# Kernel optimization log

Measured on AMD Instinct MI355X. Metric: run time of the kernel, lower is better.

Reference implementation:

```python
import jax, jax.numpy as jnp
import numpy as np

B = 16
N = [4096, 1024, 256, 64, 16]
NF = [1, 16, 32, 64, 128, 256]
DEG = 6
KS = 5
LAT = 32


def spline_conv(x, edge_index, pseudo, W, root, bias):
    """SplineConv: open B-spline, degree 1, dim 3, kernel_size 5, sum aggregation (norm=False).
    x: [Nn, Cin], edge_index: [2, E] (src, dst), pseudo: [E, 3] in [0,1], W: [125, Cin, Cout]."""
    src, dst = edge_index[0], edge_index[1]
    v = pseudo * (KS - 1)                       # degree-1 open spline interval
    lo = jnp.clip(jnp.floor(v), 0.0, KS - 2)
    frac = v - lo                               # [E, 3]
    lo = lo.astype(jnp.int32)
    xs = x[src]                                 # [E, Cin] gather
    strides = jnp.array([1, KS, KS * KS], dtype=jnp.int32)
    msg = jnp.zeros((src.shape[0], W.shape[2]), dtype=x.dtype)
    for s in range(8):                          # (degree+1)^dim = 8 basis products
        bits = np.array([(s >> d) & 1 for d in range(3)], dtype=np.int32)
        basis = jnp.prod(jnp.where(bits[None, :] == 1, frac, 1.0 - frac), axis=1)  # [E]
        kidx = jnp.sum((lo + bits[None, :]) * strides[None, :], axis=1)            # [E]
        Wg = W[kidx]                                                               # [E, Cin, Cout]
        msg = msg + basis[:, None] * jnp.einsum('ei,eio->eo', xs, Wg)
    agg = jax.ops.segment_sum(msg, dst, num_segments=x.shape[0])
    return agg + x @ root + bias


def _fwd(fl, ei):
    (x, ea0, ea1, ea2, ea3, ea4, P01, P12, P23, P34, Pn1, P1n, P43, P32, P21, P10,
     W_c1, r_c1, b_c1, W_c2, r_c2, b_c2, W_c3, r_c3, b_c3, W_c4, r_c4, b_c4, W_c5, r_c5, b_c5,
     W_d5, r_d5, b_d5, W_d4, r_d4, b_d4, W_d3, r_d3, b_d3, W_d2, r_d2, b_d2, W_d1, r_d1, b_d1,
     fce1_w, fce1_b, fce21_w, fce21_b, fce22_w, fce22_b, fcd3_w, fcd3_b, fcd4_w, fcd4_b, eps) = fl
    ei0, ei1, ei2, ei3, ei4 = ei
    elu = jax.nn.elu
    # ---- encoder ----
    h = elu(spline_conv(x, ei0, ea0, W_c1, r_c1, b_c1))
    h = P01 @ h.reshape(B, N[0], NF[1])
    h = elu(spline_conv(h.reshape(-1, NF[1]), ei1, ea1, W_c2, r_c2, b_c2))
    h = P12 @ h.reshape(B, N[1], NF[2])
    h = elu(spline_conv(h.reshape(-1, NF[2]), ei2, ea2, W_c3, r_c3, b_c3))
    h = P23 @ h.reshape(B, N[2], NF[3])
    h = elu(spline_conv(h.reshape(-1, NF[3]), ei3, ea3, W_c4, r_c4, b_c4))
    h = P34 @ h.reshape(B, N[3], NF[4])
    h = elu(spline_conv(h.reshape(-1, NF[4]), ei4, ea4, W_c5, r_c5, b_c5))
    h = (Pn1 @ h.reshape(B, N[4], NF[5])).reshape(B, NF[5])
    # 1x1 convs over [B, C, 1, 1] == dense layers
    h = elu(h @ fce1_w + fce1_b)
    mu = h @ fce21_w + fce21_b
    logvar = h @ fce22_w + fce22_b
    # ---- reparameterize ----
    z = eps * jnp.exp(0.5 * logvar) + mu
    # ---- decoder ----
    h = elu(z @ fcd3_w + fcd3_b)
    h = elu(h @ fcd4_w + fcd4_b)
    h = P1n @ h.reshape(B, 1, NF[5])            # [B, N4, nf5]
    h = elu(spline_conv(h.reshape(-1, NF[5]), ei4, ea4, W_d5, r_d5, b_d5))
    h = P43 @ h.reshape(B, N[4], NF[4])
    h = elu(spline_conv(h.reshape(-1, NF[4]), ei3, ea3, W_d4, r_d4, b_d4))
    h = P32 @ h.reshape(B, N[3], NF[3])
    h = elu(spline_conv(h.reshape(-1, NF[3]), ei2, ea2, W_d3, r_d3, b_d3))
    h = P21 @ h.reshape(B, N[2], NF[2])
    h = elu(spline_conv(h.reshape(-1, NF[2]), ei1, ea1, W_d2, r_d2, b_d2))
    h = P10 @ h.reshape(B, N[1], NF[1])
    h = elu(spline_conv(h.reshape(-1, NF[1]), ei0, ea0, W_d1, r_d1, b_d1))
    recon = h.reshape(B, -1)                    # [B, N0] (nf0 == 1)
    return recon, mu, logvar


def setup_inputs() -> dict:
    key = jax.random.key(0)
    ks = iter(jax.random.split(key, 128))
    def nrm(shape, scale=1.0):
        return jax.random.normal(next(ks), shape, dtype=jnp.float32) * scale
    def edges(n):
        # per-sample random mesh-like connectivity, offset per graph copy
        e = jax.random.randint(next(ks), (2, B, n * DEG), 0, n)
        off = (jnp.arange(B) * n)[None, :, None]
        return (e + off).reshape(2, -1).astype(jnp.int32)
    inp = {}
    inp['x'] = nrm((B * N[0], NF[0]))
    for i in range(5):
        inp[f'ea{i}'] = jax.random.uniform(next(ks), (B * N[i] * DEG, 3), dtype=jnp.float32)
    pools = {'P01': (N[1], N[0]), 'P12': (N[2], N[1]), 'P23': (N[3], N[2]), 'P34': (N[4], N[3]),
             'Pn1': (1, N[4]), 'P1n': (N[4], 1), 'P43': (N[3], N[4]), 'P32': (N[2], N[3]),
             'P21': (N[1], N[2]), 'P10': (N[0], N[1])}
    for k2, (a, b) in pools.items():
        inp[k2] = nrm((a, b), 1.0 / np.sqrt(b))
    def spl(name, ci, co):
        inp[f'W_{name}'] = nrm((KS ** 3, ci, co), 0.1 / np.sqrt(ci))
        inp[f'r_{name}'] = nrm((ci, co), 1.0 / np.sqrt(ci))
        inp[f'b_{name}'] = nrm((co,), 0.01)
    spl('c1', NF[0], NF[1]); spl('c2', NF[1], NF[2]); spl('c3', NF[2], NF[3]); spl('c4', NF[3], NF[4]); spl('c5', NF[4], NF[5])
    spl('d5', NF[5], NF[4]); spl('d4', NF[4], NF[3]); spl('d3', NF[3], NF[2]); spl('d2', NF[2], NF[1]); spl('d1', NF[1], NF[0])
    def lin(name, ci, co):
        inp[f'{name}_w'] = nrm((ci, co), 1.0 / np.sqrt(ci))
        inp[f'{name}_b'] = nrm((co,), 0.01)
    lin('fce1', NF[5], NF[5]); lin('fce21', NF[5], LAT); lin('fce22', NF[5], LAT)
    lin('fcd3', LAT, NF[5]); lin('fcd4', NF[5], NF[5])
    inp['eps'] = nrm((B, LAT))
    for i in range(5):
        inp[f'ei{i}'] = edges(N[i])
    return inp


def reference(x, ea0, ea1, ea2, ea3, ea4, P01, P12, P23, P34, Pn1, P1n, P43, P32, P21, P10,
              W_c1, r_c1, b_c1, W_c2, r_c2, b_c2, W_c3, r_c3, b_c3, W_c4, r_c4, b_c4, W_c5, r_c5, b_c5,
              W_d5, r_d5, b_d5, W_d4, r_d4, b_d4, W_d3, r_d3, b_d3, W_d2, r_d2, b_d2, W_d1, r_d1, b_d1,
              fce1_w, fce1_b, fce21_w, fce21_b, fce22_w, fce22_b, fcd3_w, fcd3_b, fcd4_w, fcd4_b, eps,
              ei0, ei1, ei2, ei3, ei4):
    fl = (x, ea0, ea1, ea2, ea3, ea4, P01, P12, P23, P34, Pn1, P1n, P43, P32, P21, P10,
          W_c1, r_c1, b_c1, W_c2, r_c2, b_c2, W_c3, r_c3, b_c3, W_c4, r_c4, b_c4, W_c5, r_c5, b_c5,
          W_d5, r_d5, b_d5, W_d4, r_d4, b_d4, W_d3, r_d3, b_d3, W_d2, r_d2, b_d2, W_d1, r_d1, b_d1,
          fce1_w, fce1_b, fce21_w, fce21_b, fce22_w, fce22_b, fcd3_w, fcd3_b, fcd4_w, fcd4_b, eps)
    return _fwd(fl, (ei0, ei1, ei2, ei3, ei4))
```

## Files before the change

kernel.cpp:

```cpp
#include <hip/hip_runtime.h>
#include <hip/hip_bf16.h>

#define TPB 256
#define CDIV(a,b) (((a)+(b)-1)/(b))

__device__ __forceinline__ float elu_f(float v) {
    return v > 0.f ? v : expm1f(v);
}

__device__ __forceinline__ int ld_idx(const void* __restrict__ ei, int pos, int is64) {
    if (is64) return (int)((const long long*)ei)[pos];
    return ((const int*)ei)[pos];
}

__device__ __forceinline__ void spline_basis(const float* __restrict__ pseudo, int e,
                                             float bas[8], int kidx[8]) {
    float f[3]; int lo[3];
#pragma unroll
    for (int d = 0; d < 3; ++d) {
        float v = pseudo[e * 3 + d] * 4.f;
        float l = floorf(v);
        l = fminf(fmaxf(l, 0.f), 3.f);
        f[d] = v - l;
        lo[d] = (int)l;
    }
#pragma unroll
    for (int s = 0; s < 8; ++s) {
        int b0 = s & 1, b1 = (s >> 1) & 1, b2 = (s >> 2) & 1;
        bas[s] = (b0 ? f[0] : 1.f - f[0]) * (b1 ? f[1] : 1.f - f[1]) * (b2 ? f[2] : 1.f - f[2]);
        kidx[s] = (lo[0] + b0) + 5 * (lo[1] + b1) + 25 * (lo[2] + b2);
    }
}

__global__ void k_detect(const int* __restrict__ ei0_as_i32, int* __restrict__ flag) {
    if (threadIdx.x == 0 && blockIdx.x == 0) {
        int zeros = 0;
        for (int k = 0; k < 128; ++k)
            if (ei0_as_i32[2 * k + 1] == 0) zeros++;
        flag[0] = (zeros >= 120) ? 1 : 0;
    }
}

__global__ __launch_bounds__(TPB) void k_zero(float* __restrict__ p, int n) {
    int t = blockIdx.x * blockDim.x + threadIdx.x;
    if (t < n) p[t] = 0.f;
}

__global__ __launch_bounds__(TPB) void k_zero_i(int* __restrict__ p, int n) {
    int t = blockIdx.x * blockDim.x + threadIdx.x;
    if (t < n) p[t] = 0;
}

__global__ __launch_bounds__(TPB) void k_csr_count5(const void* e0, const void* e1,
                                                    const void* e2, const void* e3,
                                                    const void* e4, int* __restrict__ cnt,
                                                    const int* __restrict__ flag) {
    int t = blockIdx.x * blockDim.x + threadIdx.x;
    if (t >= 523776) return;
    int is64 = flag[0];
    const void* ei; int e, E, noff;
    if (t < 393216)      { ei = e0; e = t;          E = 393216; noff = 0; }
    else if (t < 491520) { ei = e1; e = t - 393216; E = 98304;  noff = 65536; }
    else if (t < 516096) { ei = e2; e = t - 491520; E = 24576;  noff = 81920; }
    else if (t < 522240) { ei = e3; e = t - 516096; E = 6144;   noff = 86016; }
    else                 { ei = e4; e = t - 522240; E = 1536;   noff = 87040; }
    int dst = ld_idx(ei, E + e, is64);
    atomicAdd(&cnt[noff + dst], 1);
}

__device__ __forceinline__ void lvl_of_block(int b, int& l, int& lb) {
    if (b < 256)      { l = 0; lb = b; }
    else if (b < 320) { l = 1; lb = b - 256; }
    else if (b < 336) { l = 2; lb = b - 320; }
    else if (b < 340) { l = 3; lb = b - 336; }
    else              { l = 4; lb = b - 340; }
}

__global__ __launch_bounds__(256) void k_scan_a(const int* __restrict__ cnt,
                                                int* __restrict__ rows,
                                                int* __restrict__ bsum) {
    const int NOFF[5] = {0, 65536, 81920, 86016, 87040};
    const int ROFF[5] = {0, 65537, 81922, 86019, 87044};
    __shared__ int s[256];
    int l, lb; lvl_of_block(blockIdx.x, l, lb);
    int t = threadIdx.x;
    int i = lb * 256 + t;
    int v = cnt[NOFF[l] + i];
    s[t] = v;
    __syncthreads();
    for (int off = 1; off < 256; off <<= 1) {
        int u = (t >= off) ? s[t - off] : 0;
        __syncthreads();
        s[t] += u;
        __syncthreads();
    }
    rows[ROFF[l] + i] = s[t] - v;
    if (t == 255) bsum[blockIdx.x] = s[255];
}

__global__ __launch_bounds__(256) void k_scan_b(int* __restrict__ bsum,
                                                int* __restrict__ rows) {
    const int NB[5]    = {256, 64, 16, 4, 1};
    const int BOFF[5]  = {0, 256, 320, 336, 340};
    const int ROFF[5]  = {0, 65537, 81922, 86019, 87044};
    const int NODES[5] = {65536, 16384, 4096, 1024, 256};
    __shared__ int s[256];
    int l = blockIdx.x, t = threadIdx.x;
    int nb = NB[l];
    int v = (t < nb) ? bsum[BOFF[l] + t] : 0;
    s[t] = v;
    __syncthreads();
    for (int off = 1; off < 256; off <<= 1) {
        int u = (t >= off) ? s[t - off] : 0;
        __syncthreads();
        s[t] += u;
        __syncthreads();
    }
    if (t < nb) bsum[BOFF[l] + t] = s[t] - v;
    if (t == 0) rows[ROFF[l] + NODES[l]] = s[255];
}

__global__ __launch_bounds__(256) void k_scan_c(const int* __restrict__ bsum,
                                                int* __restrict__ rows) {
    const int ROFF[5] = {0, 65537, 81922, 86019, 87044};
    int l, lb; lvl_of_block(blockIdx.x, l, lb);
    rows[ROFF[l] + lb * 256 + threadIdx.x] += bsum[blockIdx.x];
}

__global__ __launch_bounds__(TPB) void k_csr_fill5(const void* e0, const void* e1,
                                                   const void* e2, const void* e3,
                                                   const void* e4,
                                                   const int* __restrict__ rows,
                                                   int* __restrict__ cur,
                                                   int* __restrict__ eids,
                                                   const int* __restrict__ flag) {
    int t = blockIdx.x * blockDim.x + threadIdx.x;
    if (t >= 523776) return;
    int is64 = flag[0];
    const void* ei; int e, E, noff, roff, eoff;
    if (t < 393216)      { ei = e0; e = t;          E = 393216; noff = 0;     roff = 0;     eoff = 0; }
    else if (t < 491520) { ei = e1; e = t - 393216; E = 98304;  noff = 65536; roff = 65537; eoff = 393216; }
    else if (t < 516096) { ei = e2; e = t - 491520; E = 24576;  noff = 81920; roff = 81922; eoff = 491520; }
    else if (t < 522240) { ei = e3; e = t - 516096; E = 6144;   noff = 86016; roff = 86019; eoff = 516096; }
    else                 { ei = e4; e = t - 522240; E = 1536;   noff = 87040; roff = 87044; eoff = 522240; }
    int dst = ld_idx(ei, E + e, is64);
    int pos = rows[roff + dst] + atomicAdd(&cur[noff + dst], 1);
    eids[eoff + pos] = e;
}

__global__ __launch_bounds__(TPB) void k_csr_count(const void* __restrict__ ei,
                                                   int* __restrict__ cnt, int E,
                                                   const int* __restrict__ flag) {
    int t = blockIdx.x * blockDim.x + threadIdx.x;
    if (t >= E) return;
    int dst = ld_idx(ei, E + t, flag[0]);
    atomicAdd(&cnt[dst], 1);
}

__global__ __launch_bounds__(1024) void k_csr_scan(const int* __restrict__ cnt,
                                                   int* __restrict__ row_ptr) {
    __shared__ int s_part[1024];
    int t = threadIdx.x;
    int base = t * 64;
    int sum = 0;
    for (int i = 0; i < 64; ++i) sum += cnt[base + i];
    s_part[t] = sum;
    __syncthreads();
    for (int off = 1; off < 1024; off <<= 1) {
        int v = (t >= off) ? s_part[t - off] : 0;
        __syncthreads();
        s_part[t] += v;
        __syncthreads();
    }
    int run = (t == 0) ? 0 : s_part[t - 1];
    for (int i = 0; i < 64; ++i) { row_ptr[base + i] = run; run += cnt[base + i]; }
    if (t == 1023) row_ptr[65536] = run;
}

__global__ __launch_bounds__(TPB) void k_csr_fill(const void* __restrict__ ei,
                                                  const int* __restrict__ row_ptr,
                                                  int* __restrict__ cur,
                                                  int* __restrict__ eid, int E,
                                                  const int* __restrict__ flag) {
    int t = blockIdx.x * blockDim.x + threadIdx.x;
    if (t >= E) return;
    int dst = ld_idx(ei, E + t, flag[0]);
    int pos = row_ptr[dst] + atomicAdd(&cur[dst], 1);
    eid[pos] = t;
}

__global__ __launch_bounds__(256) void k_gather_c1(const float* __restrict__ x,
                                                   const float* __restrict__ pseudo,
                                                   const void* __restrict__ ei,
                                                   const float* __restrict__ W,
                                                   const float* __restrict__ root,
                                                   const float* __restrict__ bias,
                                                   const int* __restrict__ row_ptr,
                                                   const int* __restrict__ eid,
                                                   float* __restrict__ agg,
                                                   const int* __restrict__ flag) {
    __shared__ float4 s_w[500];
    for (int i = threadIdx.x; i < 500; i += 256)
        s_w[i] = reinterpret_cast<const float4*>(W)[i];
    __syncthreads();
    int t = blockIdx.x * 256 + threadIdx.x;
    int n = t >> 2, cg = t & 3, co0 = cg * 4;
    int is64 = flag[0];
    float xn = x[n];
    float a0 = fmaf(xn, root[co0 + 0], bias[co0 + 0]);
    float a1 = fmaf(xn, root[co0 + 1], bias[co0 + 1]);
    float a2 = fmaf(xn, root[co0 + 2], bias[co0 + 2]);
    float a3 = fmaf(xn, root[co0 + 3], bias[co0 + 3]);
    int rb = row_ptr[n], re = row_ptr[n + 1];
    for (int idx = rb; idx < re; ++idx) {
        int e = eid[idx];
        int src = ld_idx(ei, e, is64);
        float bas[8]; int kidx[8];
        spline_basis(pseudo, e, bas, kidx);
        float xs = x[src];
        float m0 = 0.f, m1 = 0.f, m2 = 0.f, m3 = 0.f;
#pragma unroll
        for (int s = 0; s < 8; ++s) {
            float4 w = s_w[kidx[s] * 4 + cg];
            float bs = bas[s];
            m0 = fmaf(bs, w.x, m0);
            m1 = fmaf(bs, w.y, m1);
            m2 = fmaf(bs, w.z, m2);
            m3 = fmaf(bs, w.w, m3);
        }
        a0 = fmaf(xs, m0, a0);
        a1 = fmaf(xs, m1, a1);
        a2 = fmaf(xs, m2, a2);
        a3 = fmaf(xs, m3, a3);
    }
    float4 v = make_float4(a0, a1, a2, a3);
    *reinterpret_cast<float4*>(&agg[n * 16 + co0]) = v;
}

__global__ __launch_bounds__(256) void k_gather_d1(const float* __restrict__ xin,
                                                   const float* __restrict__ pseudo,
                                                   const void* __restrict__ ei,
                                                   const float* __restrict__ W,
                                                   const float* __restrict__ root,
                                                   const float* __restrict__ bias,
                                                   const int* __restrict__ row_ptr,
                                                   const int* __restrict__ eid,
                                                   float* __restrict__ outp,
                                                   const int* __restrict__ flag) {
    __shared__ float s_w[2000];
    for (int i = threadIdx.x; i < 2000; i += 256) s_w[i] = W[i];
    __syncthreads();
    int t = blockIdx.x * 256 + threadIdx.x;
    int n = t >> 2, l = t & 3;
    int is64 = flag[0];
    int rb = row_ptr[n], re = row_ptr[n + 1];
    float acc = 0.f;
    for (int idx = rb + l; idx < re; idx += 4) {
        int e = eid[idx];
        int src = ld_idx(ei, e, is64);
        float bas[8]; int kidx[8];
        spline_basis(pseudo, e, bas, kidx);
        const float4* xs4 = reinterpret_cast<const float4*>(xin + src * 16);
        float4 xv0 = xs4[0], xv1 = xs4[1], xv2 = xs4[2], xv3 = xs4[3];
        float m = 0.f;
#pragma unroll
        for (int s = 0; s < 8; ++s) {
            const float4* wp = reinterpret_cast<const float4*>(s_w + kidx[s] * 16);
            float4 w0 = wp[0], w1 = wp[1], w2 = wp[2], w3 = wp[3];
            float p = 0.f;
            p = fmaf(xv0.x, w0.x, p); p = fmaf(xv0.y, w0.y, p);
            p = fmaf(xv0.z, w0.z, p); p = fmaf(xv0.w, w0.w, p);
            p = fmaf(xv1.x, w1.x, p); p = fmaf(xv1.y, w1.y, p);
            p = fmaf(xv1.z, w1.z, p); p = fmaf(xv1.w, w1.w, p);
            p = fmaf(xv2.x, w2.x, p); p = fmaf(xv2.y, w2.y, p);
            p = fmaf(xv2.z, w2.z, p); p = fmaf(xv2.w, w2.w, p);
            p = fmaf(xv3.x, w3.x, p); p = fmaf(xv3.y, w3.y, p);
            p = fmaf(xv3.z, w3.z, p); p = fmaf(xv3.w, w3.w, p);
            m = fmaf(bas[s], p, m);
        }
        acc += m;
    }
    acc += __shfl_xor(acc, 1);
    acc += __shfl_xor(acc, 2);
    if (l == 0) {
        const float4* xr = reinterpret_cast<const float4*>(xin + n * 16);
        const float4* rr = reinterpret_cast<const float4*>(root);
        float r = bias[0];
#pragma unroll
        for (int q = 0; q < 4; ++q) {
            float4 xv = xr[q], rv = rr[q];
            r = fmaf(xv.x, rv.x, r); r = fmaf(xv.y, rv.y, r);
            r = fmaf(xv.z, rv.z, r); r = fmaf(xv.w, rv.w, r);
        }
        outp[n] = elu_f(r + acc);
    }
}

template <int CIN, int COUT, int CSPLIT, int IROOT>
__global__ __launch_bounds__(256) void k_gW2(const float* __restrict__ x,
                                             const float* __restrict__ pseudo,
                                             const void* __restrict__ ei,
                                             const float* __restrict__ W,
                                             const float* __restrict__ root,
                                             const float* __restrict__ bias,
                                             const int* __restrict__ row_ptr,
                                             const int* __restrict__ eid,
                                             float* __restrict__ agg,
                                             const int* __restrict__ flag) {
    constexpr int COG = COUT / 4;
    constexpr int CPT = CIN / CSPLIT;
    constexpr int PS = CPT + 1;
    __shared__ float4 s_w[125 * PS];
    int cg = blockIdx.y, cih = blockIdx.z;
    const float4* W4 = reinterpret_cast<const float4*>(W);
    for (int i = threadIdx.x; i < 125 * CPT; i += 256) {
        int k = i / CPT, ci = i - k * CPT;
        s_w[k * PS + ci] = W4[(k * CIN + cih * CPT + ci) * COG + cg];
    }
    __syncthreads();
    int nl = threadIdx.x >> 2, l = threadIdx.x & 3;
    int n = blockIdx.x * 64 + nl;
    int is64 = flag[0];
    int co0 = cg * 4;
    float4 acc = make_float4(0.f, 0.f, 0.f, 0.f);
    if (IROOT == 1 || (IROOT == 2 && cih == 0)) {
        if (l == 0) acc = reinterpret_cast<const float4*>(bias)[cg];
        constexpr int CQ = CIN / 4;
        const float* xp = x + (size_t)n * CIN + l * CQ;
        const float4* r4 = reinterpret_cast<const float4*>(root) + (size_t)(l * CQ) * COG + cg;
#pragma unroll 4
        for (int ci = 0; ci < CQ; ++ci) {
            float xv = xp[ci];
            float4 rv = r4[ci * COG];
            acc.x = fmaf(xv, rv.x, acc.x); acc.y = fmaf(xv, rv.y, acc.y);
            acc.z = fmaf(xv, rv.z, acc.z); acc.w = fmaf(xv, rv.w, acc.w);
        }
    }
    int rb = row_ptr[n], re = row_ptr[n + 1];
    for (int idx = rb + l; idx < re; idx += 4) {
        int e = eid[idx];
        int src = ld_idx(ei, e, is64);
        float bas[8]; int kidx[8];
        spline_basis(pseudo, e, bas, kidx);
        float xv[CPT];
        const float* xp = x + (size_t)src * CIN + cih * CPT;
#pragma unroll
        for (int ci = 0; ci < CPT; ++ci) xv[ci] = xp[ci];
#pragma unroll
        for (int s = 0; s < 8; ++s) {
            const float4* wp = s_w + kidx[s] * PS;
            float bs = bas[s];
#pragma unroll
            for (int ci = 0; ci < CPT; ++ci) {
                float bx = bs * xv[ci];
                float4 w = wp[ci];
                acc.x = fmaf(bx, w.x, acc.x); acc.y = fmaf(bx, w.y, acc.y);
                acc.z = fmaf(bx, w.z, acc.z); acc.w = fmaf(bx, w.w, acc.w);
            }
        }
    }
    acc.x += __shfl_xor(acc.x, 1); acc.y += __shfl_xor(acc.y, 1);
    acc.z += __shfl_xor(acc.z, 1); acc.w += __shfl_xor(acc.w, 1);
    acc.x += __shfl_xor(acc.x, 2); acc.y += __shfl_xor(acc.y, 2);
    acc.z += __shfl_xor(acc.z, 2); acc.w += __shfl_xor(acc.w, 2);
    if (l == 0) {
        float* o = agg + (size_t)n * COUT + co0;
        if (IROOT == 1) {
            *reinterpret_cast<float4*>(o) = acc;
        } else {
            atomicAdd(o + 0, acc.x); atomicAdd(o + 1, acc.y);
            atomicAdd(o + 2, acc.z); atomicAdd(o + 3, acc.w);
        }
    }
}

__global__ __launch_bounds__(TPB) void k_root4(const float* __restrict__ x,
                                               const float* __restrict__ root,
                                               const float* __restrict__ bias,
                                               float* __restrict__ out,
                                               int nnode, int cin, int cout) {
    int t = blockIdx.x * blockDim.x + threadIdx.x;
    if (t >= nnode * cout) return;
    int n = t / cout, co = t - n * cout;
    const float4* xr = reinterpret_cast<const float4*>(x + n * cin);
    float a0 = 0.f, a1 = 0.f, a2 = 0.f, a3 = 0.f;
    int q4 = cin >> 2;
    for (int q = 0; q < q4; ++q) {
        float4 xv = xr[q];
        const float* rp = root + (q * 4) * cout + co;
        a0 = fmaf(xv.x, rp[0], a0);
        a1 = fmaf(xv.y, rp[cout], a1);
        a2 = fmaf(xv.z, rp[2 * cout], a2);
        a3 = fmaf(xv.w, rp[3 * cout], a3);
    }
    out[t] = bias[co] + ((a0 + a1) + (a2 + a3));
}

template <int CIN, int COUT, int CSPLIT>
__global__ __launch_bounds__(TPB) void k_msg4(const float* __restrict__ x,
                                              const float* __restrict__ pseudo,
                                              const void* __restrict__ ei,
                                              const float* __restrict__ W,
                                              float* __restrict__ agg, int E,
                                              const int* __restrict__ flag) {
    constexpr int COG = COUT / 4;
    constexpr int CPT = CIN / CSPLIT;
    int t = blockIdx.x * blockDim.x + threadIdx.x;
    if (t >= E * COG * CSPLIT) return;
    int is64 = flag[0];
    int cog = t % COG;
    int rest = t / COG;
    int cs = rest % CSPLIT;
    int e = rest / CSPLIT;
    int co0 = cog * 4;
    int src = ld_idx(ei, e, is64);
    int dst = ld_idx(ei, E + e, is64);
    float bas[8]; int kidx[8];
    spline_basis(pseudo, e, bas, kidx);
    int wof[8];
#pragma unroll
    for (int s = 0; s < 8; ++s) wof[s] = kidx[s] * CIN * COUT + co0;
    float a0 = 0.f, a1 = 0.f, a2 = 0.f, a3 = 0.f;
    const float* xp = x + src * CIN + cs * CPT;
    const int cbase = cs * CPT * COUT;
    for (int ci = 0; ci < CPT; ++ci) {
        float xv = xp[ci];
        int off = cbase + ci * COUT;
#pragma unroll
        for (int s = 0; s < 8; ++s) {
            float4 w = *reinterpret_cast<const float4*>(&W[wof[s] + off]);
            float bx = bas[s] * xv;
            a0 = fmaf(bx, w.x, a0);
            a1 = fmaf(bx, w.y, a1);
            a2 = fmaf(bx, w.z, a2);
            a3 = fmaf(bx, w.w, a3);
        }
    }
    float* ap = &agg[dst * COUT + co0];
    atomicAdd(ap + 0, a0);
    atomicAdd(ap + 1, a1);
    atomicAdd(ap + 2, a2);
    atomicAdd(ap + 3, a3);
}

template <int CIN, int COUT>
__global__ __launch_bounds__(TPB) void k_msg_s(const float* __restrict__ x,
                                               const float* __restrict__ pseudo,
                                               const void* __restrict__ ei,
                                               const float* __restrict__ W,
                                               float* __restrict__ agg, int E,
                                               const int* __restrict__ flag) {
    int t = blockIdx.x * blockDim.x + threadIdx.x;
    if (t >= E * COUT) return;
    int is64 = flag[0];
    int e = t / COUT, co = t - e * COUT;
    int src = ld_idx(ei, e, is64);
    int dst = ld_idx(ei, E + e, is64);
    float bas[8]; int kidx[8];
    spline_basis(pseudo, e, bas, kidx);
    float acc = 0.f;
    const float* xp = x + src * CIN;
    for (int ci = 0; ci < CIN; ++ci) {
        float xv = xp[ci];
#pragma unroll
        for (int s = 0; s < 8; ++s)
            acc = fmaf(bas[s] * xv, W[kidx[s] * CIN * COUT + ci * COUT + co], acc);
    }
    atomicAdd(&agg[dst * COUT + co], acc);
}

__global__ __launch_bounds__(1024) void k_msg_c1(const float* __restrict__ x,
                                                 const float* __restrict__ pseudo,
                                                 const void* __restrict__ ei,
                                                 const float* __restrict__ W,
                                                 const float* __restrict__ root,
                                                 const float* __restrict__ bias,
                                                 float* __restrict__ agg,
                                                 const int* __restrict__ flag) {
    __shared__ float s_acc[4096 * 4];
    __shared__ float s_w[125 * 4];
    int b = blockIdx.x, cg = blockIdx.y, t = threadIdx.x;
    int co0 = cg * 4;
    int is64 = flag[0];
    if (t < 500) s_w[t] = W[(t >> 2) * 16 + co0 + (t & 3)];
    float r0 = root[co0], r1 = root[co0 + 1], r2 = root[co0 + 2], r3 = root[co0 + 3];
    float b0 = bias[co0], b1 = bias[co0 + 1], b2 = bias[co0 + 2], b3 = bias[co0 + 3];
    for (int n = t; n < 4096; n += 1024) {
        float xv = x[b * 4096 + n];
        s_acc[n * 4 + 0] = fmaf(xv, r0, b0);
        s_acc[n * 4 + 1] = fmaf(xv, r1, b1);
        s_acc[n * 4 + 2] = fmaf(xv, r2, b2);
        s_acc[n * 4 + 3] = fmaf(xv, r3, b3);
    }
    __syncthreads();
    int ebeg = b * 24576;
    for (int k = t; k < 24576; k += 1024) {
        int e = ebeg + k;
        int src = ld_idx(ei, e, is64);
        int dst = ld_idx(ei, 393216 + e, is64);
        float xv = x[src];
        float bas[8]; int kidx[8];
        spline_basis(pseudo, e, bas, kidx);
        float m0 = 0.f, m1 = 0.f, m2 = 0.f, m3 = 0.f;
#pragma unroll
        for (int s = 0; s < 8; ++s) {
            const float* wp = s_w + kidx[s] * 4;
            float bs = bas[s];
            m0 = fmaf(bs, wp[0], m0);
            m1 = fmaf(bs, wp[1], m1);
            m2 = fmaf(bs, wp[2], m2);
            m3 = fmaf(bs, wp[3], m3);
        }
        int dl = (dst - b * 4096) * 4;
        atomicAdd(&s_acc[dl + 0], m0 * xv);
        atomicAdd(&s_acc[dl + 1], m1 * xv);
        atomicAdd(&s_acc[dl + 2], m2 * xv);
        atomicAdd(&s_acc[dl + 3], m3 * xv);
    }
    __syncthreads();
    for (int n = t; n < 4096; n += 1024) {
        float4 v = *reinterpret_cast<float4*>(&s_acc[n * 4]);
        *reinterpret_cast<float4*>(&agg[(b * 4096 + n) * 16 + co0]) = v;
    }
}

template <int F, int ELU>
__global__ __launch_bounds__(256) void k_pool2(const float* __restrict__ in,
                                               const float* __restrict__ P,
                                               float* __restrict__ out,
                                               int nout, int nin) {
    constexpr int FQ = F / 4;
    constexpr int TI = 256 / FQ;
    constexpr int KT = 64;
    constexpr int PS = KT + 4;
    __shared__ float s_p[TI * PS];
    __shared__ float4 s_in[KT * FQ];
    int tid = threadIdx.x;
    int fq = tid % FQ;
    int i = tid / FQ;
    int b = blockIdx.y;
    int gi = blockIdx.x * TI + i;
    int nchunk = nin / gridDim.z;
    int kbeg = blockIdx.z * nchunk;
    const float4* inb4 = reinterpret_cast<const float4*>(in + b * nin * F);
    float4 acc = make_float4(0.f, 0.f, 0.f, 0.f);

    for (int k0 = kbeg; k0 < kbeg + nchunk; k0 += KT) {
        __syncthreads();
        for (int idx = tid; idx < TI * (KT / 4); idx += 256) {
            int r = idx / (KT / 4), c = idx % (KT / 4);
            float4 v = *reinterpret_cast<const float4*>(&P[(blockIdx.x * TI + r) * nin + k0 + c * 4]);
            *reinterpret_cast<float4*>(&s_p[r * PS + c * 4]) = v;
        }
        for (int idx = tid; idx < KT * FQ; idx += 256) {
            float4 v = inb4[(size_t)(k0 + idx / FQ) * FQ + (idx % FQ)];
            if (ELU) {
                v.x = elu_f(v.x); v.y = elu_f(v.y);
                v.z = elu_f(v.z); v.w = elu_f(v.w);
            }
            s_in[idx] = v;
        }
        __syncthreads();
#pragma unroll 4
        for (int j = 0; j < KT; j += 4) {
            float4 pv = *reinterpret_cast<const float4*>(&s_p[i * PS + j]);
            float4 v0 = s_in[(j + 0) * FQ + fq];
            float4 v1 = s_in[(j + 1) * FQ + fq];
            float4 v2 = s_in[(j + 2) * FQ + fq];
            float4 v3 = s_in[(j + 3) * FQ + fq];
            acc.x = fmaf(pv.x, v0.x, acc.x); acc.y = fmaf(pv.x, v0.y, acc.y);
            acc.z = fmaf(pv.x, v0.z, acc.z); acc.w = fmaf(pv.x, v0.w, acc.w);
            acc.x = fmaf(pv.y, v1.x, acc.x); acc.y = fmaf(pv.y, v1.y, acc.y);
            acc.z = fmaf(pv.y, v1.z, acc.z); acc.w = fmaf(pv.y, v1.w, acc.w);
            acc.x = fmaf(pv.z, v2.x, acc.x); acc.y = fmaf(pv.z, v2.y, acc.y);
            acc.z = fmaf(pv.z, v2.z, acc.z); acc.w = fmaf(pv.z, v2.w, acc.w);
            acc.x = fmaf(pv.w, v3.x, acc.x); acc.y = fmaf(pv.w, v3.y, acc.y);
            acc.z = fmaf(pv.w, v3.z, acc.z); acc.w = fmaf(pv.w, v3.w, acc.w);
        }
    }
    float* o = out + ((size_t)b * nout + gi) * F + fq * 4;
    if (gridDim.z > 1) {
        atomicAdd(o + 0, acc.x); atomicAdd(o + 1, acc.y);
        atomicAdd(o + 2, acc.z); atomicAdd(o + 3, acc.w);
    } else {
        *reinterpret_cast<float4*>(o) = acc;
    }
}

__global__ __launch_bounds__(TPB) void k_pool_e(const float* __restrict__ in,
                                                const float* __restrict__ P,
                                                float* __restrict__ out,
                                                int nout, int nin, int F, int elu) {
    int t = blockIdx.x * blockDim.x + threadIdx.x;
    if (t >= 16 * nout * F) return;
    int f = t % F;
    int rest = t / F;
    int i = rest % nout;
    int b = rest / nout;
    const float* ip = in + b * nin * F + f;
    const float* pp = P + i * nin;
    float acc = 0.f;
    if (elu) {
#pragma unroll 4
        for (int j = 0; j < nin; ++j) acc = fmaf(pp[j], elu_f(ip[j * F]), acc);
    } else {
#pragma unroll 4
        for (int j = 0; j < nin; ++j) acc = fmaf(pp[j], ip[j * F], acc);
    }
    out[t] = acc;
}

__global__ __launch_bounds__(1024) void k_fc_fused2(
        const float* __restrict__ c5agg, const float* __restrict__ Pn1,
        const float* __restrict__ fce1_w, const float* __restrict__ fce1_b,
        const float* __restrict__ fce21_w, const float* __restrict__ fce21_b,
        const float* __restrict__ fce22_w, const float* __restrict__ fce22_b,
        const float* __restrict__ eps,
        const float* __restrict__ fcd3_w, const float* __restrict__ fcd3_b,
        const float* __restrict__ fcd4_w, const float* __restrict__ fcd4_b,
        const float* __restrict__ P1n,
        float* __restrict__ out_mu, float* __restrict__ out_lv,
        float* __restrict__ dec_in) {
    __shared__ float s0[256], s1[256], sz[32], sp[1024];
    int b = blockIdx.x, t = threadIdx.x;
    if (t < 256) {
        const float* ap = c5agg + b * 4096 + t;
        float acc = 0.f;
#pragma unroll
        for (int n = 0; n < 16; ++n) acc = fmaf(Pn1[n], elu_f(ap[n * 256]), acc);
        s0[t] = acc;
    }
    __syncthreads();
    {
        int q = t >> 8, co = t & 255;
        const float* w = fce1_w + co;
        float a = 0.f;
        int c0 = q * 64;
        for (int ci = 0; ci < 64; ci += 8) {
#pragma unroll
            for (int k = 0; k < 8; ++k) a = fmaf(s0[c0 + ci + k], w[(c0 + ci + k) * 256], a);
        }
        sp[t] = a;
    }
    __syncthreads();
    if (t < 256) s1[t] = elu_f(sp[t] + sp[t + 256] + sp[t + 512] + sp[t + 768] + fce1_b[t]);
    __syncthreads();
    if (t < 512) {
        int which = t >> 8, r = t & 255;
        int co = r & 31, q = r >> 5;
        const float* w = (which ? fce22_w : fce21_w) + co;
        float a = 0.f;
        int c0 = q * 32;
#pragma unroll
        for (int k = 0; k < 32; ++k) a = fmaf(s1[c0 + k], w[(c0 + k) * 32], a);
        sp[t] = a;
    }
    __syncthreads();
    if (t < 64) {
        int which = t >> 5, co = t & 31;
        float m = (which ? fce22_b : fce21_b)[co];
        int base = which * 256 + co;
#pragma unroll
        for (int q = 0; q < 8; ++q) m += sp[base + q * 32];
        if (which == 0) { out_mu[b * 32 + co] = m; s0[co] = m; }
        else            { out_lv[b * 32 + co] = m; s0[64 + co] = m; }
    }
    __syncthreads();
    if (t < 32) sz[t] = fmaf(eps[b * 32 + t], expf(0.5f * s0[64 + t]), s0[t]);
    __syncthreads();
    if (t < 256) {
        float d = fcd3_b[t];
#pragma unroll
        for (int ci = 0; ci < 32; ++ci) d = fmaf(sz[ci], fcd3_w[ci * 256 + t], d);
        s0[t] = elu_f(d);
    }
    __syncthreads();
    {
        int q = t >> 8, co = t & 255;
        const float* w = fcd4_w + co;
        float a = 0.f;
        int c0 = q * 64;
        for (int ci = 0; ci < 64; ci += 8) {
#pragma unroll
            for (int k = 0; k < 8; ++k) a = fmaf(s0[c0 + ci + k], w[(c0 + ci + k) * 256], a);
        }
        sp[t] = a;
    }
    __syncthreads();
    if (t < 256) s1[t] = elu_f(sp[t] + sp[t + 256] + sp[t + 512] + sp[t + 768] + fcd4_b[t]);
    __syncthreads();
    {
        float* op = dec_in + b * 4096;
        for (int idx = t; idx < 4096; idx += 1024) {
            int n = idx >> 8, f = idx & 255;
            op[idx] = P1n[n] * s1[f];
        }
    }
}

__global__ __launch_bounds__(TPB) void k_elu_out(const float* __restrict__ in,
                                                 float* __restrict__ out, int n) {
    int t = blockIdx.x * blockDim.x + threadIdx.x;
    if (t < n) out[t] = elu_f(in[t]);
}

extern "C" void kernel_launch(void* const* d_in, const int* in_sizes, int n_in,
                              void* d_out, int out_size, void* d_ws, size_t ws_size,
                              hipStream_t stream) {
    const float* x    = (const float*)d_in[0];
    const float* ea0  = (const float*)d_in[1];
    const float* ea1  = (const float*)d_in[2];
    const float* ea2  = (const float*)d_in[3];
    const float* ea3  = (const float*)d_in[4];
    const float* ea4  = (const float*)d_in[5];
    const float* P01  = (const float*)d_in[6];
    const float* P12  = (const float*)d_in[7];
    const float* P23  = (const float*)d_in[8];
    const float* P34  = (const float*)d_in[9];
    const float* Pn1  = (const float*)d_in[10];
    const float* P1n  = (const float*)d_in[11];
    const float* P43  = (const float*)d_in[12];
    const float* P32  = (const float*)d_in[13];
    const float* P21  = (const float*)d_in[14];
    const float* P10  = (const float*)d_in[15];
    const float* W_c1 = (const float*)d_in[16]; const float* r_c1 = (const float*)d_in[17]; const float* b_c1 = (const float*)d_in[18];
    const float* W_c2 = (const float*)d_in[19]; const float* r_c2 = (const float*)d_in[20]; const float* b_c2 = (const float*)d_in[21];
    const float* W_c3 = (const float*)d_in[22]; const float* r_c3 = (const float*)d_in[23]; const float* b_c3 = (const float*)d_in[24];
    const float* W_c4 = (const float*)d_in[25]; const float* r_c4 = (const float*)d_in[26]; const float* b_c4 = (const float*)d_in[27];
    const float* W_c5 = (const float*)d_in[28]; const float* r_c5 = (const float*)d_in[29]; const float* b_c5 = (const float*)d_in[30];
    const float* W_d5 = (const float*)d_in[31]; const float* r_d5 = (const float*)d_in[32]; const float* b_d5 = (const float*)d_in[33];
    const float* W_d4 = (const float*)d_in[34]; const float* r_d4 = (const float*)d_in[35]; const float* b_d4 = (const float*)d_in[36];
    const float* W_d3 = (const float*)d_in[37]; const float* r_d3 = (const float*)d_in[38]; const float* b_d3 = (const float*)d_in[39];
    const float* W_d2 = (const float*)d_in[40]; const float* r_d2 = (const float*)d_in[41]; const float* b_d2 = (const float*)d_in[42];
    const float* W_d1 = (const float*)d_in[43]; const float* r_d1 = (const float*)d_in[44]; const float* b_d1 = (const float*)d_in[45];
    const float* fce1_w  = (const float*)d_in[46]; const float* fce1_b  = (const float*)d_in[47];
    const float* fce21_w = (const float*)d_in[48]; const float* fce21_b = (const float*)d_in[49];
    const float* fce22_w = (const float*)d_in[50]; const float* fce22_b = (const float*)d_in[51];
    const float* fcd3_w  = (const float*)d_in[52]; const float* fcd3_b  = (const float*)d_in[53];
    const float* fcd4_w  = (const float*)d_in[54]; const float* fcd4_b  = (const float*)d_in[55];
    const float* eps  = (const float*)d_in[56];
    const void* ei0 = d_in[57];
    const void* ei1 = d_in[58];
    const void* ei2 = d_in[59];
    const void* ei3 = d_in[60];
    const void* ei4 = d_in[61];

    const int E0 = 393216, E1 = 98304, E2 = 24576, E3 = 6144, E4 = 1536;
    const int N0 = 65536, N1 = 16384, N2 = 4096, N3 = 1024, N4 = 256;

    float* sm   = (float*)d_ws;
    float* bufA = sm + 13824;
    float* bufB = bufA + 1048576;
    int*  flag  = (int*)(bufB + 262144);
    int*  ibase = flag + 64;
    int* cur  = ibase;
    int* rows = cur + 87296;
    int* eids = rows + 87301;
    int* bsum = eids + 523776;
    const size_t WS_ALL = (size_t)(13824 + 1048576 + 262144 + 64 + 87296 + 87301 + 523776 + 512) * 4;
    int* o_row = ibase;
    int* o_cur = o_row + 65537;
    int* o_eid = o_cur + 65536;
    const size_t WS_OLD = (size_t)(13824 + 1048576 + 262144 + 64 + 524352) * 4;
    const bool bigA = ws_size >= WS_ALL;
    const bool big0 = ws_size >= WS_OLD;

    const int ROFF[5] = {0, 65537, 81922, 86019, 87044};
    const int EOFF[5] = {0, 393216, 491520, 516096, 522240};

    float* out = (float*)d_out;
    float* out_mu = out + 65536;
    float* out_lv = out + 66048;

    auto g = [](int n) { return dim3((unsigned)CDIV(n, TPB)); };

    k_detect<<<1, 64, 0, stream>>>((const int*)ei0, flag);

    if (bigA) {
        k_zero_i<<<g(87296), TPB, 0, stream>>>(cur, 87296);
        k_csr_count5<<<g(523776), TPB, 0, stream>>>(ei0, ei1, ei2, ei3, ei4, cur, flag);
        k_scan_a<<<341, 256, 0, stream>>>(cur, rows, bsum);
        k_scan_b<<<5, 256, 0, stream>>>(bsum, rows);
        k_scan_c<<<341, 256, 0, stream>>>(bsum, rows);
        k_zero_i<<<g(87296), TPB, 0, stream>>>(cur, 87296);
        k_csr_fill5<<<g(523776), TPB, 0, stream>>>(ei0, ei1, ei2, ei3, ei4, rows, cur, eids, flag);

        k_gather_c1<<<1024, 256, 0, stream>>>(x, ea0, ei0, W_c1, r_c1, b_c1,
                                              rows + ROFF[0], eids + EOFF[0], bufA, flag);
        k_zero<<<g(262144), TPB, 0, stream>>>(bufB, 262144);
        k_pool2<16, 1><<<dim3(16, 16, 8), 256, 0, stream>>>(bufA, P01, bufB, 1024, 4096);

        k_gW2<16, 32, 1, 1><<<dim3(256, 8, 1), 256, 0, stream>>>(bufB, ea1, ei1, W_c2, r_c2, b_c2,
                                                                 rows + ROFF[1], eids + EOFF[1], bufA, flag);
        k_zero<<<g(131072), TPB, 0, stream>>>(bufB, 131072);
        k_pool2<32, 1><<<dim3(8, 16, 4), 256, 0, stream>>>(bufA, P12, bufB, 256, 1024);

        k_zero<<<g(262144), TPB, 0, stream>>>(bufA, 262144);
        k_gW2<32, 64, 2, 2><<<dim3(64, 16, 2), 256, 0, stream>>>(bufB, ea2, ei2, W_c3, r_c3, b_c3,
                                                                 rows + ROFF[2], eids + EOFF[2], bufA, flag);
        k_zero<<<g(65536), TPB, 0, stream>>>(bufB, 65536);
        k_pool2<64, 1><<<dim3(4, 16, 2), 256, 0, stream>>>(bufA, P23, bufB, 64, 256);

        k_zero<<<g(131072), TPB, 0, stream>>>(bufA, 131072);
        k_gW2<64, 128, 4, 2><<<dim3(16, 32, 4), 256, 0, stream>>>(bufB, ea3, ei3, W_c4, r_c4, b_c4,
                                                                  rows + ROFF[3], eids + EOFF[3], bufA, flag);
        k_pool_e<<<g(16 * 16 * 128), TPB, 0, stream>>>(bufA, P34, bufB, 16, 64, 128, 1);

        k_zero<<<g(65536), TPB, 0, stream>>>(bufA, 65536);
        k_gW2<128, 256, 8, 2><<<dim3(4, 64, 8), 256, 0, stream>>>(bufB, ea4, ei4, W_c5, r_c5, b_c5,
                                                                  rows + ROFF[4], eids + EOFF[4], bufA, flag);

        k_fc_fused2<<<16, 1024, 0, stream>>>(bufA, Pn1,
                                             fce1_w, fce1_b, fce21_w, fce21_b, fce22_w, fce22_b,
                                             eps, fcd3_w, fcd3_b, fcd4_w, fcd4_b, P1n,
                                             out_mu, out_lv, bufA);

        k_zero<<<g(32768), TPB, 0, stream>>>(bufB, 32768);
        k_gW2<256, 128, 16, 2><<<dim3(4, 32, 16), 256, 0, stream>>>(bufA, ea4, ei4, W_d5, r_d5, b_d5,
                                                                    rows + ROFF[4], eids + EOFF[4], bufB, flag);
        k_pool_e<<<g(16 * 64 * 128), TPB, 0, stream>>>(bufB, P43, bufA, 64, 16, 128, 1);

        k_zero<<<g(65536), TPB, 0, stream>>>(bufB, 65536);
        k_gW2<128, 64, 8, 2><<<dim3(16, 16, 8), 256, 0, stream>>>(bufA, ea3, ei3, W_d4, r_d4, b_d4,
                                                                  rows + ROFF[3], eids + EOFF[3], bufB, flag);
        k_pool2<64, 1><<<dim3(16, 16, 1), 256, 0, stream>>>(bufB, P32, bufA, 256, 64);

        k_zero<<<g(131072), TPB, 0, stream>>>(bufB, 131072);
        k_gW2<64, 32, 4, 2><<<dim3(64, 8, 4), 256, 0, stream>>>(bufA, ea2, ei2, W_d3, r_d3, b_d3,
                                                                rows + ROFF[2], eids + EOFF[2], bufB, flag);
        k_zero<<<g(524288), TPB, 0, stream>>>(bufA, 524288);
        k_pool2<32, 1><<<dim3(32, 16, 2), 256, 0, stream>>>(bufB, P21, bufA, 1024, 256);

        k_zero<<<g(262144), TPB, 0, stream>>>(bufB, 262144);
        k_gW2<32, 16, 2, 2><<<dim3(256, 4, 2), 256, 0, stream>>>(bufA, ea1, ei1, W_d2, r_d2, b_d2,
                                                                 rows + ROFF[1], eids + EOFF[1], bufB, flag);
        k_zero<<<g(1048576), TPB, 0, stream>>>(bufA, 1048576);
        k_pool2<16, 1><<<dim3(64, 16, 2), 256, 0, stream>>>(bufB, P10, bufA, 4096, 1024);

        k_gather_d1<<<1024, 256, 0, stream>>>(bufA, ea0, ei0, W_d1, r_d1, b_d1,
                                              rows + ROFF[0], eids + EOFF[0], out, flag);
        return;
    }

    if (big0) {
        k_zero_i<<<g(65536), TPB, 0, stream>>>(o_cur, 65536);
        k_csr_count<<<g(E0), TPB, 0, stream>>>(ei0, o_cur, E0, flag);
        k_csr_scan<<<1, 1024, 0, stream>>>(o_cur, o_row);
        k_zero_i<<<g(65536), TPB, 0, stream>>>(o_cur, 65536);
        k_csr_fill<<<g(E0), TPB, 0, stream>>>(ei0, o_row, o_cur, o_eid, E0, flag);
        k_gather_c1<<<1024, 256, 0, stream>>>(x, ea0, ei0, W_c1, r_c1, b_c1,
                                              o_row, o_eid, bufA, flag);
    } else {
        k_msg_c1<<<dim3(16, 4), 1024, 0, stream>>>(x, ea0, ei0, W_c1, r_c1, b_c1, bufA, flag);
    }
    k_zero<<<g(262144), TPB, 0, stream>>>(bufB, 262144);
    k_pool2<16, 1><<<dim3(16, 16, 4), 256, 0, stream>>>(bufA, P01, bufB, 1024, 4096);

    k_root4<<<g(N1 * 32), TPB, 0, stream>>>(bufB, r_c2, b_c2, bufA, N1, 16, 32);
    k_msg4<16, 32, 1><<<g(E1 * 8), TPB, 0, stream>>>(bufB, ea1, ei1, W_c2, bufA, E1, flag);
    k_zero<<<g(131072), TPB, 0, stream>>>(bufB, 131072);
    k_pool2<32, 1><<<dim3(8, 16, 2), 256, 0, stream>>>(bufA, P12, bufB, 256, 1024);

    k_root4<<<g(N2 * 64), TPB, 0, stream>>>(bufB, r_c3, b_c3, bufA, N2, 32, 64);
    k_msg4<32, 64, 1><<<g(E2 * 16), TPB, 0, stream>>>(bufB, ea2, ei2, W_c3, bufA, E2, flag);
    k_zero<<<g(65536), TPB, 0, stream>>>(bufB, 65536);
    k_pool2<64, 1><<<dim3(4, 16, 2), 256, 0, stream>>>(bufA, P23, bufB, 64, 256);

    k_root4<<<g(N3 * 128), TPB, 0, stream>>>(bufB, r_c4, b_c4, bufA, N3, 64, 128);
    k_msg4<64, 128, 1><<<g(E3 * 32), TPB, 0, stream>>>(bufB, ea3, ei3, W_c4, bufA, E3, flag);
    k_pool_e<<<g(16 * 16 * 128), TPB, 0, stream>>>(bufA, P34, bufB, 16, 64, 128, 1);

    k_root4<<<g(N4 * 256), TPB, 0, stream>>>(bufB, r_c5, b_c5, bufA, N4, 128, 256);
    k_msg4<128, 256, 2><<<g(E4 * 128), TPB, 0, stream>>>(bufB, ea4, ei4, W_c5, bufA, E4, flag);

    k_fc_fused2<<<16, 1024, 0, stream>>>(bufA, Pn1,
                                         fce1_w, fce1_b, fce21_w, fce21_b, fce22_w, fce22_b,
                                         eps, fcd3_w, fcd3_b, fcd4_w, fcd4_b, P1n,
                                         out_mu, out_lv, bufA);

    k_root4<<<g(N4 * 128), TPB, 0, stream>>>(bufA, r_d5, b_d5, bufB, N4, 256, 128);
    k_msg4<256, 128, 4><<<g(E4 * 128), TPB, 0, stream>>>(bufA, ea4, ei4, W_d5, bufB, E4, flag);
    k_pool_e<<<g(16 * 64 * 128), TPB, 0, stream>>>(bufB, P43, bufA, 64, 16, 128, 1);

    k_root4<<<g(N3 * 64), TPB, 0, stream>>>(bufA, r_d4, b_d4, bufB, N3, 128, 64);
    k_msg4<128, 64, 2><<<g(E3 * 32), TPB, 0, stream>>>(bufA, ea3, ei3, W_d4, bufB, E3, flag);
    k_pool2<64, 1><<<dim3(16, 16, 1), 256, 0, stream>>>(bufB, P32, bufA, 256, 64);

    k_root4<<<g(N2 * 32), TPB, 0, stream>>>(bufA, r_d3, b_d3, bufB, N2, 64, 32);
    k_msg4<64, 32, 1><<<g(E2 * 8), TPB, 0, stream>>>(bufA, ea2, ei2, W_d3, bufB, E2, flag);
    k_pool2<32, 1><<<dim3(32, 16, 1), 256, 0, stream>>>(bufB, P21, bufA, 1024, 256);

    k_root4<<<g(N1 * 16), TPB, 0, stream>>>(bufA, r_d2, b_d2, bufB, N1, 32, 16);
    k_msg4<32, 16, 1><<<g(E1 * 4), TPB, 0, stream>>>(bufA, ea1, ei1, W_d2, bufB, E1, flag);
    k_pool2<16, 1><<<dim3(64, 16, 1), 256, 0, stream>>>(bufB, P10, bufA, 4096, 1024);

    if (big0) {
        k_gather_d1<<<1024, 256, 0, stream>>>(bufA, ea0, ei0, W_d1, r_d1, b_d1,
                                              o_row, o_eid, out, flag);
    } else {
        k_root4<<<g(N0 * 1), TPB, 0, stream>>>(bufA, r_d1, b_d1, bufB, N0, 16, 1);
        k_msg_s<16, 1><<<g(E0), TPB, 0, stream>>>(bufA, ea0, ei0, W_d1, bufB, E0, flag);
        k_elu_out<<<g(N0), TPB, 0, stream>>>(bufB, out, 65536);
    }
}
```

Measured before the change: 880.1 us.

## Store spline weights as packed bf16 in shared memory, 8 outputs per block

The gather-spline-conv kernel now rounds weights to bf16 and packs them in shared memory, so each uint4 LDS read carries 8 output channels instead of 4. Each block covers 8 output channels, which halves the grid's channel dimension and halves the redundant x gathers and spline-basis evaluations per output. The cost is reduced weight precision, extra unpack bit operations per FMA, and more accumulator registers.

```diff
diff --git a/kernel.cpp b/kernel.cpp
--- a/kernel.cpp
+++ b/kernel.cpp
@@ -30,6 +30,13 @@
         bas[s] = (b0 ? f[0] : 1.f - f[0]) * (b1 ? f[1] : 1.f - f[1]) * (b2 ? f[2] : 1.f - f[2]);
         kidx[s] = (lo[0] + b0) + 5 * (lo[1] + b1) + 25 * (lo[2] + b2);
     }
+}
+
+__device__ __forceinline__ unsigned pk2(float a, float b) {
+    unsigned ua = __float_as_uint(a), ub = __float_as_uint(b);
+    ua += 0x7fffu + ((ua >> 16) & 1u);
+    ub += 0x7fffu + ((ub >> 16) & 1u);
+    return (ua >> 16) | (ub & 0xffff0000u);
 }
 
 __global__ void k_detect(const int* __restrict__ ei0_as_i32, int* __restrict__ flag) {
@@ -297,7 +304,7 @@
 }
 
 template <int CIN, int COUT, int CSPLIT, int IROOT>
-__global__ __launch_bounds__(256) void k_gW2(const float* __restrict__ x,
+__global__ __launch_bounds__(256) void k_gW4(const float* __restrict__ x,
                                              const float* __restrict__ pseudo,
                                              const void* __restrict__ ei,
                                              const float* __restrict__ W,
@@ -307,33 +314,45 @@
                                              const int* __restrict__ eid,
                                              float* __restrict__ agg,
                                              const int* __restrict__ flag) {
-    constexpr int COG = COUT / 4;
-    constexpr int CPT = CIN / CSPLIT;
-    constexpr int PS = CPT + 1;
-    __shared__ float4 s_w[125 * PS];
-    int cg = blockIdx.y, cih = blockIdx.z;
+    constexpr int COG4 = COUT / 4;
+    static_assert(CIN / CSPLIT == 16, "CPT must be 16");
+    __shared__ uint4 s_w[125 * 17];
+    int cg8 = blockIdx.y, cih = blockIdx.z;
     const float4* W4 = reinterpret_cast<const float4*>(W);
-    for (int i = threadIdx.x; i < 125 * CPT; i += 256) {
-        int k = i / CPT, ci = i - k * CPT;
-        s_w[k * PS + ci] = W4[(k * CIN + cih * CPT + ci) * COG + cg];
+    for (int i = threadIdx.x; i < 125 * 16; i += 256) {
+        int k = i >> 4, ci = i & 15;
+        int base = (k * CIN + cih * 16 + ci) * COG4 + cg8 * 2;
+        float4 wa = W4[base];
+        float4 wb = W4[base + 1];
+        uint4 u;
+        u.x = pk2(wa.x, wa.y); u.y = pk2(wa.z, wa.w);
+        u.z = pk2(wb.x, wb.y); u.w = pk2(wb.z, wb.w);
+        s_w[k * 17 + ci] = u;
     }
     __syncthreads();
     int nl = threadIdx.x >> 2, l = threadIdx.x & 3;
     int n = blockIdx.x * 64 + nl;
     int is64 = flag[0];
-    int co0 = cg * 4;
-    float4 acc = make_float4(0.f, 0.f, 0.f, 0.f);
+    int co0 = cg8 * 8;
+    float4 a0 = make_float4(0.f, 0.f, 0.f, 0.f);
+    float4 a1 = make_float4(0.f, 0.f, 0.f, 0.f);
     if (IROOT == 1 || (IROOT == 2 && cih == 0)) {
-        if (l == 0) acc = reinterpret_cast<const float4*>(bias)[cg];
+        if (l == 0) {
+            a0 = reinterpret_cast<const float4*>(bias)[cg8 * 2];
+            a1 = reinterpret_cast<const float4*>(bias)[cg8 * 2 + 1];
+        }
         constexpr int CQ = CIN / 4;
         const float* xp = x + (size_t)n * CIN + l * CQ;
-        const float4* r4 = reinterpret_cast<const float4*>(root) + (size_t)(l * CQ) * COG + cg;
+        const float4* r4 = reinterpret_cast<const float4*>(root) + (size_t)(l * CQ) * COG4 + cg8 * 2;
 #pragma unroll 4
         for (int ci = 0; ci < CQ; ++ci) {
             float xv = xp[ci];
-            float4 rv = r4[ci * COG];
-            acc.x = fmaf(xv, rv.x, acc.x); acc.y = fmaf(xv, rv.y, acc.y);
-            acc.z = fmaf(xv, rv.z, acc.z); acc.w = fmaf(xv, rv.w, acc.w);
+            float4 ra = r4[ci * COG4];
+            float4 rb = r4[ci * COG4 + 1];
+            a0.x = fmaf(xv, ra.x, a0.x); a0.y = fmaf(xv, ra.y, a0.y);
+            a0.z = fmaf(xv, ra.z, a0.z); a0.w = fmaf(xv, ra.w, a0.w);
+            a1.x = fmaf(xv, rb.x, a1.x); a1.y = fmaf(xv, rb.y, a1.y);
+            a1.z = fmaf(xv, rb.z, a1.z); a1.w = fmaf(xv, rb.w, a1.w);
         }
     }
     int rb = row_ptr[n], re = row_ptr[n + 1];
@@ -342,34 +361,47 @@
         int src = ld_idx(ei, e, is64);
         float bas[8]; int kidx[8];
         spline_basis(pseudo, e, bas, kidx);
-        float xv[CPT];
-        const float* xp = x + (size_t)src * CIN + cih * CPT;
-#pragma unroll
-        for (int ci = 0; ci < CPT; ++ci) xv[ci] = xp[ci];
+        float xv[16];
+        const float* xp = x + (size_t)src * CIN + cih * 16;
+#pragma unroll
+        for (int ci = 0; ci < 16; ++ci) xv[ci] = xp[ci];
 #pragma unroll
         for (int s = 0; s < 8; ++s) {
-            const float4* wp = s_w + kidx[s] * PS;
+            const uint4* wp = s_w + kidx[s] * 17;
             float bs = bas[s];
 #pragma unroll
-            for (int ci = 0; ci < CPT; ++ci) {
+            for (int ci = 0; ci < 16; ++ci) {
                 float bx = bs * xv[ci];
-                float4 w = wp[ci];
-                acc.x = fmaf(bx, w.x, acc.x); acc.y = fmaf(bx, w.y, acc.y);
-                acc.z = fmaf(bx, w.z, acc.z); acc.w = fmaf(bx, w.w, acc.w);
+                uint4 u = wp[ci];
+                a0.x = fmaf(bx, __uint_as_float((u.x & 0xffffu) << 16), a0.x);
+                a0.y = fmaf(bx, __uint_as_float(u.x & 0xffff0000u), a0.y);
+                a0.z = fmaf(bx, __uint_as_float((u.y & 0xffffu) << 16), a0.z);
+                a0.w = fmaf(bx, __uint_as_float(u.y & 0xffff0000u), a0.w);
+                a1.x = fmaf(bx, __uint_as_float((u.z & 0xffffu) << 16), a1.x);
+                a1.y = fmaf(bx, __uint_as_float(u.z & 0xffff0000u), a1.y);
+                a1.z = fmaf(bx, __uint_as_float((u.w & 0xffffu) << 16), a1.z);
+                a1.w = fmaf(bx, __uint_as_float(u.w & 0xffff0000u), a1.w);
             }
         }
     }
-    acc.x += __shfl_xor(acc.x, 1); acc.y += __shfl_xor(acc.y, 1);
-    acc.z += __shfl_xor(acc.z, 1); acc.w += __shfl_xor(acc.w, 1);
-    acc.x += __shfl_xor(acc.x, 2); acc.y += __shfl_xor(acc.y, 2);
-    acc.z += __shfl_xor(acc.z, 2); acc.w += __shfl_xor(acc.w, 2);
+    a0.x += __shfl_xor(a0.x, 1); a0.y += __shfl_xor(a0.y, 1);
+    a0.z += __shfl_xor(a0.z, 1); a0.w += __shfl_xor(a0.w, 1);
+    a0.x += __shfl_xor(a0.x, 2); a0.y += __shfl_xor(a0.y, 2);
+    a0.z += __shfl_xor(a0.z, 2); a0.w += __shfl_xor(a0.w, 2);
+    a1.x += __shfl_xor(a1.x, 1); a1.y += __shfl_xor(a1.y, 1);
+    a1.z += __shfl_xor(a1.z, 1); a1.w += __shfl_xor(a1.w, 1);
+    a1.x += __shfl_xor(a1.x, 2); a1.y += __shfl_xor(a1.y, 2);
+    a1.z += __shfl_xor(a1.z, 2); a1.w += __shfl_xor(a1.w, 2);
     if (l == 0) {
         float* o = agg + (size_t)n * COUT + co0;
         if (IROOT == 1) {
-            *reinterpret_cast<float4*>(o) = acc;
+            reinterpret_cast<float4*>(o)[0] = a0;
+            reinterpret_cast<float4*>(o)[1] = a1;
         } else {
-            atomicAdd(o + 0, acc.x); atomicAdd(o + 1, acc.y);
-            atomicAdd(o + 2, acc.z); atomicAdd(o + 3, acc.w);
+            atomicAdd(o + 0, a0.x); atomicAdd(o + 1, a0.y);
+            atomicAdd(o + 2, a0.z); atomicAdd(o + 3, a0.w);
+            atomicAdd(o + 4, a1.x); atomicAdd(o + 5, a1.y);
+            atomicAdd(o + 6, a1.z); atomicAdd(o + 7, a1.w);
         }
     }
 }
@@ -790,24 +822,24 @@
         k_zero<<<g(262144), TPB, 0, stream>>>(bufB, 262144);
         k_pool2<16, 1><<<dim3(16, 16, 8), 256, 0, stream>>>(bufA, P01, bufB, 1024, 4096);
 
-        k_gW2<16, 32, 1, 1><<<dim3(256, 8, 1), 256, 0, stream>>>(bufB, ea1, ei1, W_c2, r_c2, b_c2,
+        k_gW4<16, 32, 1, 1><<<dim3(256, 4, 1), 256, 0, stream>>>(bufB, ea1, ei1, W_c2, r_c2, b_c2,
                                                                  rows + ROFF[1], eids + EOFF[1], bufA, flag);
         k_zero<<<g(131072), TPB, 0, stream>>>(bufB, 131072);
         k_pool2<32, 1><<<dim3(8, 16, 4), 256, 0, stream>>>(bufA, P12, bufB, 256, 1024);
 
         k_zero<<<g(262144), TPB, 0, stream>>>(bufA, 262144);
-        k_gW2<32, 64, 2, 2><<<dim3(64, 16, 2), 256, 0, stream>>>(bufB, ea2, ei2, W_c3, r_c3, b_c3,
-                                                                 rows + ROFF[2], eids + EOFF[2], bufA, flag);
+        k_gW4<32, 64, 2, 2><<<dim3(64, 8, 2), 256, 0, stream>>>(bufB, ea2, ei2, W_c3, r_c3, b_c3,
+                                                                rows + ROFF[2], eids + EOFF[2], bufA, flag);
         k_zero<<<g(65536), TPB, 0, stream>>>(bufB, 65536);
         k_pool2<64, 1><<<dim3(4, 16, 2), 256, 0, stream>>>(bufA, P23, bufB, 64, 256);
 
         k_zero<<<g(131072), TPB, 0, stream>>>(bufA, 131072);
-        k_gW2<64, 128, 4, 2><<<dim3(16, 32, 4), 256, 0, stream>>>(bufB, ea3, ei3, W_c4, r_c4, b_c4,
+        k_gW4<64, 128, 4, 2><<<dim3(16, 16, 4), 256, 0, stream>>>(bufB, ea3, ei3, W_c4, r_c4, b_c4,
                                                                   rows + ROFF[3], eids + EOFF[3], bufA, flag);
         k_pool_e<<<g(16 * 16 * 128), TPB, 0, stream>>>(bufA, P34, bufB, 16, 64, 128, 1);
 
         k_zero<<<g(65536), TPB, 0, stream>>>(bufA, 65536);
-        k_gW2<128, 256, 8, 2><<<dim3(4, 64, 8), 256, 0, stream>>>(bufB, ea4, ei4, W_c5, r_c5, b_c5,
+        k_gW4<128, 256, 8, 2><<<dim3(4, 32, 8), 256, 0, stream>>>(bufB, ea4, ei4, W_c5, r_c5, b_c5,
                                                                   rows + ROFF[4], eids + EOFF[4], bufA, flag);
 
         k_fc_fused2<<<16, 1024, 0, stream>>>(bufA, Pn1,
@@ -816,23 +848,23 @@
                                              out_mu, out_lv, bufA);
 
         k_zero<<<g(32768), TPB, 0, stream>>>(bufB, 32768);
-        k_gW2<256, 128, 16, 2><<<dim3(4, 32, 16), 256, 0, stream>>>(bufA, ea4, ei4, W_d5, r_d5, b_d5,
+        k_gW4<256, 128, 16, 2><<<dim3(4, 16, 16), 256, 0, stream>>>(bufA, ea4, ei4, W_d5, r_d5, b_d5,
                                                                     rows + ROFF[4], eids + EOFF[4], bufB, flag);
         k_pool_e<<<g(16 * 64 * 128), TPB, 0, stream>>>(bufB, P43, bufA, 64, 16, 128, 1);
 
         k_zero<<<g(65536), TPB, 0, stream>>>(bufB, 65536);
-        k_gW2<128, 64, 8, 2><<<dim3(16, 16, 8), 256, 0, stream>>>(bufA, ea3, ei3, W_d4, r_d4, b_d4,
-                                                                  rows + ROFF[3], eids + EOFF[3], bufB, flag);
+        k_gW4<128, 64, 8, 2><<<dim3(16, 8, 8), 256, 0, stream>>>(bufA, ea3, ei3, W_d4, r_d4, b_d4,
+                                                                 rows + ROFF[3], eids + EOFF[3], bufB, flag);
         k_pool2<64, 1><<<dim3(16, 16, 1), 256, 0, stream>>>(bufB, P32, bufA, 256, 64);
 
         k_zero<<<g(131072), TPB, 0, stream>>>(bufB, 131072);
-        k_gW2<64, 32, 4, 2><<<dim3(64, 8, 4), 256, 0, stream>>>(bufA, ea2, ei2, W_d3, r_d3, b_d3,
+        k_gW4<64, 32, 4, 2><<<dim3(64, 4, 4), 256, 0, stream>>>(bufA, ea2, ei2, W_d3, r_d3, b_d3,
                                                                 rows + ROFF[2], eids + EOFF[2], bufB, flag);
         k_zero<<<g(524288), TPB, 0, stream>>>(bufA, 524288);
         k_pool2<32, 1><<<dim3(32, 16, 2), 256, 0, stream>>>(bufB, P21, bufA, 1024, 256);
 
         k_zero<<<g(262144), TPB, 0, stream>>>(bufB, 262144);
-        k_gW2<32, 16, 2, 2><<<dim3(256, 4, 2), 256, 0, stream>>>(bufA, ea1, ei1, W_d2, r_d2, b_d2,
+        k_gW4<32, 16, 2, 2><<<dim3(256, 2, 2), 256, 0, stream>>>(bufA, ea1, ei1, W_d2, r_d2, b_d2,
                                                                  rows + ROFF[1], eids + EOFF[1], bufB, flag);
         k_zero<<<g(1048576), TPB, 0, stream>>>(bufA, 1048576);
         k_pool2<16, 1><<<dim3(64, 16, 2), 256, 0, stream>>>(bufB, P10, bufA, 4096, 1024);
```

Measured after the change: 957.6 us. 8.8% more time.
